# Kernel tuning notes

Hardware: AMD Instinct MI355X
Metric: run time of the kernel (lower is better)

## Reference

```python
import jax, jax.numpy as jnp
import numpy as np

LAM = 0.95

def setup_inputs() -> dict:
    key = jax.random.key(0)
    d2 = jax.random.normal(key, (16, 8192, 256), dtype=jnp.float32)
    return {"d2": d2}

def reference(d2) -> jnp.ndarray:
    # z_t = lam * z_{t-1} + (1 - lam) * d2_t, scanned over time axis L
    B, L, K = d2.shape
    lam = jnp.asarray(LAM, d2.dtype)
    one_minus = jnp.asarray(1.0 - LAM, d2.dtype)

    def step(z, x):  # z: [B,K], x: [B,K]
        z = lam * z + one_minus * x
        return z, z

    z0 = jnp.zeros((B, K), dtype=d2.dtype)
    _, z = jax.lax.scan(step, z0, jnp.swapaxes(d2, 0, 1))  # [L,B,K]
    return jnp.swapaxes(z, 0, 1)  # [B,L,K]
```

## Files before the change

### kernel.cpp

```cpp
#include <hip/hip_runtime.h>


#define LAM   0.95f
#define CHUNK 128
#define WARM  128
#define UNROLL 16

constexpr int B  = 16;
constexpr int L  = 8192;
constexpr int K  = 256;
constexpr int G  = L / CHUNK;
constexpr int KS = 4;

__global__ __launch_bounds__(256) void ewma_kernel(const float* __restrict__ x,
                                                   float* __restrict__ out) {
    const int wib  = (int)(threadIdx.x >> 6);
    const int lane = threadIdx.x & 63;
    const int j    = blockIdx.x & (G - 1);
    const int b    = blockIdx.x >> 6;
    const int s    = j * CHUNK;
    const int t0   = (j == 0) ? 0 : (s - WARM);

    const long chan = (long)b * L * K + wib * 64 + lane;
    const float* __restrict__ pin  = x   + chan + (long)t0 * K;
    float*       __restrict__ pout = out + chan + (long)t0 * K;

    const float c = 1.0f - LAM;
    float z = 0.f;

    const int total      = (s + CHUNK) - t0;
    const int tiles      = total / UNROLL;
    const int warm_tiles = (s - t0) / UNROLL;

    float bufA[UNROLL], bufB[UNROLL];

    auto load_tile = [&](float (&buf)[UNROLL], int t) {
        const float* __restrict__ p = pin + (long)t * UNROLL * K;
        #pragma unroll
        for (int u = 0; u < UNROLL; ++u) buf[u] = p[(long)u * K];
    };

    auto comp_tile = [&](float (&buf)[UNROLL], int t) {
        float* __restrict__ p = pout + (long)t * UNROLL * K;
        const bool st = (t >= warm_tiles);
        #pragma unroll
        for (int u = 0; u < UNROLL; ++u) {
            z = fmaf(LAM, z, c * buf[u]);
            if (st) __builtin_nontemporal_store(z, &p[(long)u * K]);
        }
    };

    load_tile(bufA, 0);
    for (int t = 0; t < tiles; t += 2) {
        load_tile(bufB, t + 1);
        comp_tile(bufA, t);
        if (t + 2 < tiles) load_tile(bufA, t + 2);
        comp_tile(bufB, t + 1);
    }
}

extern "C" void kernel_launch(void* const* d_in, const int* in_sizes, int n_in,
                              void* d_out, int out_size, void* d_ws, size_t ws_size,
                              hipStream_t stream) {
    const float* x = (const float*)d_in[0];
    float* out = (float*)d_out;

    const int blocks = B * G;
    hipLaunchKernelGGL(ewma_kernel, dim3(blocks), dim3(256), 0, stream, x, out);
}
```

Baseline: 249.6 us.

## Stage input tiles into LDS via async global_load_lds double buffering

Replaces the register double-buffered loads with asynchronous global-to-LDS loads (global_load_lds) into a per-wave two-slot LDS ring. Explicit vmcnt waits let the scan on one tile overlap the loads for the next two tiles. This is meant to keep more memory requests in flight and cut VGPR pressure. The cost is LDS reads on the critical path and fragile hand-counted vmcnt values that mix loads and nontemporal stores.

```diff
diff --git a/kernel.cpp b/kernel.cpp
--- a/kernel.cpp
+++ b/kernel.cpp
@@ -1,19 +1,29 @@
 #include <hip/hip_runtime.h>
 
 
-#define LAM   0.95f
-#define CHUNK 128
-#define WARM  128
-#define UNROLL 16
+#define LAM    0.95f
+#define CHUNK  128
+#define WARM   128
+#define TSTEPS 16
 
-constexpr int B  = 16;
-constexpr int L  = 8192;
-constexpr int K  = 256;
-constexpr int G  = L / CHUNK;
-constexpr int KS = 4;
+constexpr int B = 16;
+constexpr int L = 8192;
+constexpr int K = 256;
+constexpr int G = L / CHUNK;
+
+typedef const __attribute__((address_space(1))) unsigned int gu32;
+typedef __attribute__((address_space(3)))       unsigned int lu32;
+
+#define WAITV(N)                                                   \
+    do {                                                           \
+        asm volatile("s_waitcnt vmcnt(" #N ")" ::: "memory");      \
+        __builtin_amdgcn_sched_barrier(0);                         \
+    } while (0)
 
 __global__ __launch_bounds__(256) void ewma_kernel(const float* __restrict__ x,
                                                    float* __restrict__ out) {
+    __shared__ float lds[4][2][TSTEPS][64];
+
     const int wib  = (int)(threadIdx.x >> 6);
     const int lane = threadIdx.x & 63;
     const int j    = blockIdx.x & (G - 1);
@@ -29,34 +39,46 @@
     float z = 0.f;
 
     const int total      = (s + CHUNK) - t0;
-    const int tiles      = total / UNROLL;
-    const int warm_tiles = (s - t0) / UNROLL;
+    const int NT         = total / TSTEPS;
+    const int warm_tiles = (s - t0) / TSTEPS;
 
-    float bufA[UNROLL], bufB[UNROLL];
-
-    auto load_tile = [&](float (&buf)[UNROLL], int t) {
-        const float* __restrict__ p = pin + (long)t * UNROLL * K;
+    auto stage = [&](int tile) {
+        const float* p = pin + (long)tile * TSTEPS * K;
+        lu32* lp = (lu32*)&lds[wib][tile & 1][0][0];
         #pragma unroll
-        for (int u = 0; u < UNROLL; ++u) buf[u] = p[(long)u * K];
+        for (int u = 0; u < TSTEPS; ++u)
+            __builtin_amdgcn_global_load_lds((gu32*)(p + (long)u * K),
+                                             lp + (long)u * 64, 4, 0, 0);
     };
 
-    auto comp_tile = [&](float (&buf)[UNROLL], int t) {
-        float* __restrict__ p = pout + (long)t * UNROLL * K;
-        const bool st = (t >= warm_tiles);
+    auto consume = [&](int tile) {
+        const bool st = (tile >= warm_tiles);
+        float* p = pout + (long)tile * TSTEPS * K;
         #pragma unroll
-        for (int u = 0; u < UNROLL; ++u) {
-            z = fmaf(LAM, z, c * buf[u]);
+        for (int u = 0; u < TSTEPS; ++u) {
+            const float xv = lds[wib][tile & 1][u][lane];
+            z = fmaf(LAM, z, c * xv);
             if (st) __builtin_nontemporal_store(z, &p[(long)u * K]);
         }
     };
 
-    load_tile(bufA, 0);
-    for (int t = 0; t < tiles; t += 2) {
-        load_tile(bufB, t + 1);
-        comp_tile(bufA, t);
-        if (t + 2 < tiles) load_tile(bufA, t + 2);
-        comp_tile(bufB, t + 1);
+    stage(0);
+    stage(1);
+
+    const int W1 = warm_tiles + 1;
+    int i = 0;
+    for (; i < W1; ++i) {
+        WAITV(16);
+        consume(i);
+        if (i + 2 < NT) stage(i + 2);
     }
+    for (; i < NT - 1; ++i) {
+        WAITV(32);
+        consume(i);
+        if (i + 2 < NT) stage(i + 2);
+    }
+    WAITV(16);
+    consume(NT - 1);
 }
 
 extern "C" void kernel_launch(void* const* d_in, const int* in_sizes, int n_in,
```

Result: no change. 247.7 us (-0.7%).
